# Performance work log

Measured on AMD Instinct MI355X. Metric: run time of the kernel, lower is better.

## Reference

```python
import jax, jax.numpy as jnp
import numpy as np

N = 50000      # points
K = 16         # neighbors per point
DIM = 256      # channels
H = 8          # heads
HD = DIM // H  # head dim


def setup_inputs() -> dict:
    key = jax.random.key(0)
    ks = jax.random.split(key, 8)
    feats = jax.random.normal(ks[0], (N, DIM), jnp.float32)
    xyz = jax.random.normal(ks[1], (N, 3), jnp.float32)
    # sorted segment ids: each point attends to exactly K neighbors
    index_0 = jnp.repeat(jnp.arange(N, dtype=jnp.int32), K)            # [M]
    index_1 = jax.random.randint(ks[2], (N * K,), 0, N, dtype=jnp.int32)  # [M]
    index_0_offsets = jnp.arange(N + 1, dtype=jnp.int32) * K
    s = 1.0 / np.sqrt(DIM)
    qkv_w = jax.random.normal(ks[3], (3 * DIM, DIM), jnp.float32) * s
    qkv_b = jax.random.normal(ks[4], (3 * DIM,), jnp.float32) * 0.01
    proj_w = jax.random.normal(ks[5], (DIM, DIM), jnp.float32) * s
    proj_b = jax.random.normal(ks[6], (DIM,), jnp.float32) * 0.01
    return {
        'feats': feats, 'xyz': xyz,
        'index_0': index_0, 'index_1': index_1,
        'index_0_offsets': index_0_offsets, 'n_max': K,
        'qkv_w': qkv_w, 'qkv_b': qkv_b, 'proj_w': proj_w, 'proj_b': proj_b,
    }


def reference(feats, xyz, index_0, index_1, index_0_offsets, n_max,
              qkv_w, qkv_b, proj_w, proj_b):
    n, c = feats.shape
    scale = (c // H) ** (-0.5)
    qkv = (feats @ qkv_w.T + qkv_b).reshape(n, 3, H, HD)  # [N,3,H,HD]
    q = qkv[:, 0] * scale
    k = qkv[:, 1]
    v = qkv[:, 2]
    # attention_step1: per-pair gathered dot product -> [M, H]
    attn = jnp.einsum('mhd,mhd->mh', q[index_0], k[index_1])
    # scatter_softmax over segments of index_0 (numerically stable)
    seg_max = jax.ops.segment_max(attn, index_0, num_segments=n)  # [N,H]
    e = jnp.exp(attn - seg_max[index_0])
    denom = jax.ops.segment_sum(e, index_0, num_segments=n)       # [N,H]
    attn = e / denom[index_0]                                     # [M,H]
    # attention_step2: scatter weighted sum of gathered values -> [N,H,HD]
    x = jax.ops.segment_sum(attn[:, :, None] * v[index_1], index_0,
                            num_segments=n)
    x = x.reshape(n, c)
    return x @ proj_w.T + proj_b
```

## Files before the change

kernel.cpp:

```cpp
#include <hip/hip_runtime.h>
#include <hip/hip_bf16.h>
#include <stdint.h>

typedef __bf16 bf16x8_t __attribute__((ext_vector_type(8)));
typedef float f32x4_t __attribute__((ext_vector_type(4)));

__device__ __forceinline__ float b2f(unsigned short u) {
    union { uint32_t i; float f; } x; x.i = ((uint32_t)u) << 16; return x.f;
}
__device__ __forceinline__ unsigned short f2b(float f) {
    union { float f; uint32_t i; } x; x.f = f;
    uint32_t r = (x.i + 0x7fffu + ((x.i >> 16) & 1u)) >> 16;
    return (unsigned short)r;
}

__global__ void cvt_f32_bf16(const float* __restrict__ in, unsigned short* __restrict__ out, int n) {
    int i = (blockIdx.x * blockDim.x + threadIdx.x) * 4;
    if (i >= n) return;
    const float4 v = *reinterpret_cast<const float4*>(in + i);
    ushort4 o;
    o.x = f2b(v.x); o.y = f2b(v.y); o.z = f2b(v.z); o.w = f2b(v.w);
    *reinterpret_cast<ushort4*>(out + i) = o;
}

template <bool OUT_BF16>
__launch_bounds__(256, 2)
__global__ void gemm_bf16(const unsigned short* __restrict__ A,
                          const unsigned short* __restrict__ W,
                          const float* __restrict__ bias,
                          void* __restrict__ Cout,
                          int M, int Nn, int Kk) {
    __shared__ unsigned short As[128 * 64];
    __shared__ unsigned short Bs[128 * 64];
    const int t = threadIdx.x;
    const int w = t >> 6;
    const int l = t & 63;
    const int blockRow = blockIdx.y * 128;
    const int blockCol = blockIdx.x * 128;
    const int wm = w >> 1, wn = w & 1;

    f32x4_t acc[4][4];
#pragma unroll
    for (int i = 0; i < 4; ++i)
#pragma unroll
        for (int j = 0; j < 4; ++j) acc[i][j] = (f32x4_t)0.f;

    const int srow = t >> 3;
    const int scol = (t & 7) * 8;

    for (int k0 = 0; k0 < Kk; k0 += 64) {
#pragma unroll
        for (int c = 0; c < 4; ++c) {
            int arow = blockRow + c * 32 + srow;
            arow = arow < M ? arow : M - 1;
            const unsigned short* ga = A + (size_t)arow * Kk + k0 + scol;
            const int brow = blockCol + c * 32 + srow;
            const unsigned short* gb = W + (size_t)brow * Kk + k0 + scol;
            unsigned short* la = &As[c * 2048 + w * 512];
            unsigned short* lb = &Bs[c * 2048 + w * 512];
            __builtin_amdgcn_global_load_lds((const __attribute__((address_space(1))) void*)ga,
                                             (__attribute__((address_space(3))) void*)la, 16, 0, 0);
            __builtin_amdgcn_global_load_lds((const __attribute__((address_space(1))) void*)gb,
                                             (__attribute__((address_space(3))) void*)lb, 16, 0, 0);
        }
        __syncthreads();
#pragma unroll
        for (int kc = 0; kc < 2; ++kc) {
            bf16x8_t af[4], bfr[4];
            const int kof = kc * 32 + (l >> 4) * 8;
#pragma unroll
            for (int i = 0; i < 4; ++i) {
                af[i]  = *reinterpret_cast<const bf16x8_t*>(&As[(wm * 64 + i * 16 + (l & 15)) * 64 + kof]);
                bfr[i] = *reinterpret_cast<const bf16x8_t*>(&Bs[(wn * 64 + i * 16 + (l & 15)) * 64 + kof]);
            }
#pragma unroll
            for (int i = 0; i < 4; ++i)
#pragma unroll
                for (int j = 0; j < 4; ++j)
                    acc[i][j] = __builtin_amdgcn_mfma_f32_16x16x32_bf16(af[i], bfr[j], acc[i][j], 0, 0, 0);
        }
        __syncthreads();
    }

    const int lr = (l >> 4) * 4;
    const int lc = l & 15;
#pragma unroll
    for (int i = 0; i < 4; ++i) {
#pragma unroll
        for (int j = 0; j < 4; ++j) {
            const int col = blockCol + wn * 64 + j * 16 + lc;
            const float bz = bias[col];
#pragma unroll
            for (int r = 0; r < 4; ++r) {
                const int row = blockRow + wm * 64 + i * 16 + lr + r;
                if (row < M) {
                    const float val = acc[i][j][r] + bz;
                    if (OUT_BF16)
                        ((unsigned short*)Cout)[(size_t)row * Nn + col] = f2b(val);
                    else
                        ((float*)Cout)[(size_t)row * Nn + col] = val;
                }
            }
        }
    }
}

__global__ void attn_bf16(const unsigned short* __restrict__ qkv,
                          const int* __restrict__ index_1,
                          unsigned short* __restrict__ x) {
    const int w = threadIdx.x >> 6;
    const int i = blockIdx.x * 4 + w;
    const int l = threadIdx.x & 63;
    const int h = l >> 3;
    const int d0 = (l & 7) * 4;
    const float scale = 0.17677669529663687f;

    const ushort4 qu = *reinterpret_cast<const ushort4*>(&qkv[(size_t)i * 768 + h * 32 + d0]);
    float qx = b2f(qu.x) * scale, qy = b2f(qu.y) * scale,
          qz = b2f(qu.z) * scale, qw = b2f(qu.w) * scale;

    int nbr[16];
#pragma unroll
    for (int m = 0; m < 16; ++m) nbr[m] = index_1[i * 16 + m];

    float s[16];
#pragma unroll
    for (int m = 0; m < 16; ++m) {
        const ushort4 ku = *reinterpret_cast<const ushort4*>(&qkv[(size_t)nbr[m] * 768 + 256 + h * 32 + d0]);
        float p = qx * b2f(ku.x) + qy * b2f(ku.y) + qz * b2f(ku.z) + qw * b2f(ku.w);
        p += __shfl_xor(p, 1, 8);
        p += __shfl_xor(p, 2, 8);
        p += __shfl_xor(p, 4, 8);
        s[m] = p;
    }
    float mx = -1e30f;
#pragma unroll
    for (int m = 0; m < 16; ++m) mx = fmaxf(mx, s[m]);
    float sum = 0.f;
#pragma unroll
    for (int m = 0; m < 16; ++m) { s[m] = __expf(s[m] - mx); sum += s[m]; }
    const float inv = 1.f / sum;

    float ax = 0.f, ay = 0.f, az = 0.f, aw = 0.f;
#pragma unroll
    for (int m = 0; m < 16; ++m) {
        const ushort4 vu = *reinterpret_cast<const ushort4*>(&qkv[(size_t)nbr[m] * 768 + 512 + h * 32 + d0]);
        const float wt = s[m] * inv;
        ax += wt * b2f(vu.x); ay += wt * b2f(vu.y);
        az += wt * b2f(vu.z); aw += wt * b2f(vu.w);
    }
    ushort4 o;
    o.x = f2b(ax); o.y = f2b(ay); o.z = f2b(az); o.w = f2b(aw);
    *reinterpret_cast<ushort4*>(&x[(size_t)i * 256 + h * 32 + d0]) = o;
}

extern "C" void kernel_launch(void* const* d_in, const int* in_sizes, int n_in,
                              void* d_out, int out_size, void* d_ws, size_t ws_size,
                              hipStream_t stream) {
    const float* feats   = (const float*)d_in[0];
    const int*   index_1 = (const int*)d_in[3];
    const float* qkv_w   = (const float*)d_in[6];
    const float* qkv_b   = (const float*)d_in[7];
    const float* proj_w  = (const float*)d_in[8];
    const float* proj_b  = (const float*)d_in[9];
    float* out = (float*)d_out;

    const int N = 50000, DIM = 256, QKVD = 768;

    unsigned short* featsb = (unsigned short*)d_ws;
    unsigned short* qkvwb  = featsb + (size_t)N * DIM;
    unsigned short* projwb = qkvwb + (size_t)QKVD * DIM;
    unsigned short* qkvb   = projwb + (size_t)DIM * DIM;
    unsigned short* xb     = qkvb + (size_t)N * QKVD;

    cvt_f32_bf16<<<(N * DIM / 4 + 255) / 256, 256, 0, stream>>>(feats, featsb, N * DIM);
    cvt_f32_bf16<<<(QKVD * DIM / 4 + 255) / 256, 256, 0, stream>>>(qkv_w, qkvwb, QKVD * DIM);
    cvt_f32_bf16<<<(DIM * DIM / 4 + 255) / 256, 256, 0, stream>>>(proj_w, projwb, DIM * DIM);

    {
        dim3 grid(QKVD / 128, (N + 127) / 128), block(256);
        gemm_bf16<true><<<grid, block, 0, stream>>>(featsb, qkvwb, qkv_b, qkvb, N, QKVD, DIM);
    }
    attn_bf16<<<N / 4, 256, 0, stream>>>(qkvb, index_1, xb);
    {
        dim3 grid(DIM / 128, (N + 127) / 128), block(256);
        gemm_bf16<false><<<grid, block, 0, stream>>>(xb, projwb, proj_b, out, N, DIM, DIM);
    }
}
```

Before: 314.5 us.

## Remap GEMM blocks XCD-aware and prefetch all K/V gathers up front in attention

The GEMM grid is flattened to 1D and remapped so that consecutive block IDs, which go round-robin across the 8 XCDs, keep the same row tile on one XCD while sweeping column tiles. This aims to improve L2 reuse of the A rows. The row count is padded to a multiple of 8, and padded blocks exit early. In the attention kernel, all 16 neighbor K and V vectors are loaded into registers before any compute, so more gather loads are in flight and latency overlaps. The cost is higher register pressure.

Measured after the change: 309.7 us. No clear change (-1.5%).

```diff
diff --git a/kernel.cpp b/kernel.cpp
--- a/kernel.cpp
+++ b/kernel.cpp
@@ -30,13 +30,22 @@
                           const float* __restrict__ bias,
                           void* __restrict__ Cout,
                           int M, int Nn, int Kk) {
+    const int nCol = Nn >> 7;
+    const int p = blockIdx.x;
+    const int xcd = p & 7;
+    const int q = p >> 3;
+    const int c = q % nCol;
+    const int rr = q / nCol;
+    const int r = rr * 8 + xcd;
+    const int blockRow = r * 128;
+    if (blockRow >= M) return;
+    const int blockCol = c * 128;
+
     __shared__ unsigned short As[128 * 64];
     __shared__ unsigned short Bs[128 * 64];
     const int t = threadIdx.x;
     const int w = t >> 6;
     const int l = t & 63;
-    const int blockRow = blockIdx.y * 128;
-    const int blockCol = blockIdx.x * 128;
     const int wm = w >> 1, wn = w & 1;
 
     f32x4_t acc[4][4];
@@ -50,14 +59,14 @@
 
     for (int k0 = 0; k0 < Kk; k0 += 64) {
 #pragma unroll
-        for (int c = 0; c < 4; ++c) {
-            int arow = blockRow + c * 32 + srow;
+        for (int cc = 0; cc < 4; ++cc) {
+            int arow = blockRow + cc * 32 + srow;
             arow = arow < M ? arow : M - 1;
             const unsigned short* ga = A + (size_t)arow * Kk + k0 + scol;
-            const int brow = blockCol + c * 32 + srow;
+            const int brow = blockCol + cc * 32 + srow;
             const unsigned short* gb = W + (size_t)brow * Kk + k0 + scol;
-            unsigned short* la = &As[c * 2048 + w * 512];
-            unsigned short* lb = &Bs[c * 2048 + w * 512];
+            unsigned short* la = &As[cc * 2048 + w * 512];
+            unsigned short* lb = &Bs[cc * 2048 + w * 512];
             __builtin_amdgcn_global_load_lds((const __attribute__((address_space(1))) void*)ga,
                                              (__attribute__((address_space(3))) void*)la, 16, 0, 0);
             __builtin_amdgcn_global_load_lds((const __attribute__((address_space(1))) void*)gb,
@@ -91,10 +100,10 @@
             const int col = blockCol + wn * 64 + j * 16 + lc;
             const float bz = bias[col];
 #pragma unroll
-            for (int r = 0; r < 4; ++r) {
-                const int row = blockRow + wm * 64 + i * 16 + lr + r;
+            for (int rg = 0; rg < 4; ++rg) {
+                const int row = blockRow + wm * 64 + i * 16 + lr + rg;
                 if (row < M) {
-                    const float val = acc[i][j][r] + bz;
+                    const float val = acc[i][j][rg] + bz;
                     if (OUT_BF16)
                         ((unsigned short*)Cout)[(size_t)row * Nn + col] = f2b(val);
                     else
@@ -115,19 +124,27 @@
     const int d0 = (l & 7) * 4;
     const float scale = 0.17677669529663687f;
 
+    int nbr[16];
+#pragma unroll
+    for (int m = 0; m < 16; ++m) nbr[m] = index_1[i * 16 + m];
+
+    ushort4 kreg[16], vreg[16];
+#pragma unroll
+    for (int m = 0; m < 16; ++m) {
+        const unsigned short* base = qkv + (size_t)nbr[m] * 768 + 256 + h * 32 + d0;
+        kreg[m] = *reinterpret_cast<const ushort4*>(base);
+        vreg[m] = *reinterpret_cast<const ushort4*>(base + 256);
+    }
+
     const ushort4 qu = *reinterpret_cast<const ushort4*>(&qkv[(size_t)i * 768 + h * 32 + d0]);
-    float qx = b2f(qu.x) * scale, qy = b2f(qu.y) * scale,
-          qz = b2f(qu.z) * scale, qw = b2f(qu.w) * scale;
-
-    int nbr[16];
-#pragma unroll
-    for (int m = 0; m < 16; ++m) nbr[m] = index_1[i * 16 + m];
+    const float qx = b2f(qu.x) * scale, qy = b2f(qu.y) * scale,
+                qz = b2f(qu.z) * scale, qw = b2f(qu.w) * scale;
 
     float s[16];
 #pragma unroll
     for (int m = 0; m < 16; ++m) {
-        const ushort4 ku = *reinterpret_cast<const ushort4*>(&qkv[(size_t)nbr[m] * 768 + 256 + h * 32 + d0]);
-        float p = qx * b2f(ku.x) + qy * b2f(ku.y) + qz * b2f(ku.z) + qw * b2f(ku.w);
+        float p = qx * b2f(kreg[m].x) + qy * b2f(kreg[m].y)
+                + qz * b2f(kreg[m].z) + qw * b2f(kreg[m].w);
         p += __shfl_xor(p, 1, 8);
         p += __shfl_xor(p, 2, 8);
         p += __shfl_xor(p, 4, 8);
@@ -144,10 +161,9 @@
     float ax = 0.f, ay = 0.f, az = 0.f, aw = 0.f;
 #pragma unroll
     for (int m = 0; m < 16; ++m) {
-        const ushort4 vu = *reinterpret_cast<const ushort4*>(&qkv[(size_t)nbr[m] * 768 + 512 + h * 32 + d0]);
         const float wt = s[m] * inv;
-        ax += wt * b2f(vu.x); ay += wt * b2f(vu.y);
-        az += wt * b2f(vu.z); aw += wt * b2f(vu.w);
+        ax += wt * b2f(vreg[m].x); ay += wt * b2f(vreg[m].y);
+        az += wt * b2f(vreg[m].z); aw += wt * b2f(vreg[m].w);
     }
     ushort4 o;
     o.x = f2b(ax); o.y = f2b(ay); o.z = f2b(az); o.w = f2b(aw);
@@ -177,13 +193,10 @@
     cvt_f32_bf16<<<(QKVD * DIM / 4 + 255) / 256, 256, 0, stream>>>(qkv_w, qkvwb, QKVD * DIM);
     cvt_f32_bf16<<<(DIM * DIM / 4 + 255) / 256, 256, 0, stream>>>(proj_w, projwb, DIM * DIM);
 
-    {
-        dim3 grid(QKVD / 128, (N + 127) / 128), block(256);
-        gemm_bf16<true><<<grid, block, 0, stream>>>(featsb, qkvwb, qkv_b, qkvb, N, QKVD, DIM);
-    }
+    const int nRow = (N + 127) / 128;
+    const int nRowPad = ((nRow + 7) / 8) * 8;
+
+    gemm_bf16<true><<<nRowPad * (QKVD / 128), 256, 0, stream>>>(featsb, qkvwb, qkv_b, qkvb, N, QKVD, DIM);
     attn_bf16<<<N / 4, 256, 0, stream>>>(qkvb, index_1, xb);
-    {
-        dim3 grid(DIM / 128, (N + 127) / 128), block(256);
-        gemm_bf16<false><<<grid, block, 0, stream>>>(xb, projwb, proj_b, out, N, DIM, DIM);
-    }
-}
+    gemm_bf16<false><<<nRowPad * (DIM / 128), 256, 0, stream>>>(xb, projwb, proj_b, out, N, DIM, DIM);
+}
```
